# Kernel optimization log

Hardware: AMD Instinct MI355X
Metric: run time of the kernel (lower is better)

## Reference

```python
import jax, jax.numpy as jnp
import numpy as np

N = 100_000   # nodes
E = 1_600_000 # edges (avg degree 16)
D = 128       # in_dim
H = 128       # hidden_dim


def _glorot(key, shape):
    s = 1.0 / np.sqrt(shape[0])
    return jax.random.uniform(key, shape, jnp.float32, -s, s)


def setup_inputs() -> dict:
    key = jax.random.key(0)
    ks = jax.random.split(key, 8)
    x = jax.random.normal(ks[0], (N, D), jnp.float32)
    edge_index = jax.random.randint(ks[1], (2, E), 0, N)
    return {
        "x": x,
        "edge_index": edge_index,
        "Wn0": _glorot(ks[2], (D, H)),
        "Wr0": _glorot(ks[3], (D, H)),
        "b0": jnp.zeros((H,), jnp.float32),
        "Wn1": _glorot(ks[4], (H, H)),
        "Wr1": _glorot(ks[5], (H, H)),
        "b1": jnp.zeros((H,), jnp.float32),
        "Wh": _glorot(ks[6], (H, 1)),
        "bh": jnp.zeros((1,), jnp.float32),
    }


def _mean_agg(h, src, dst, n):
    # mean of source-node features scattered onto destination nodes
    summed = jax.ops.segment_sum(h[src], dst, num_segments=n)  # [N, F]
    cnt = jax.ops.segment_sum(jnp.ones((src.shape[0],), h.dtype), dst,
                              num_segments=n)
    return summed / jnp.maximum(cnt, 1.0)[:, None]


def _sage_layer(h, src, dst, Wn, Wr, b):
    # PyG SAGEConv (mean aggr): lin_l(mean_neighbors) + lin_r(root) + bias
    agg = _mean_agg(h, src, dst, h.shape[0])
    return agg @ Wn + h @ Wr + b


def reference(x, edge_index, Wn0, Wr0, b0, Wn1, Wr1, b1, Wh, bh):
    src, dst = edge_index[0], edge_index[1]
    h = jax.nn.relu(_sage_layer(x, src, dst, Wn0, Wr0, b0))  # dropout = identity (eval)
    h = jax.nn.relu(_sage_layer(h, src, dst, Wn1, Wr1, b1))
    logits = (h @ Wh + bh)[:, 0]  # squeeze(-1) -> [N]
    return logits
```

## Files before the change

kernel.cpp:

```cpp
#include <hip/hip_runtime.h>

#define THREADS 256
#define SCAN_ITEMS 8
#define NSB 128
#define BKT_MAX 3200
#define CHUNK 1024

typedef float f32x4 __attribute__((ext_vector_type(4)));
typedef __bf16 bf16x8 __attribute__((ext_vector_type(8)));
typedef int intx4 __attribute__((ext_vector_type(4)));

__device__ inline unsigned short f32_to_bf16_rne(float f) {
    unsigned int u = __float_as_uint(f);
    unsigned int r = u + 0x7fffu + ((u >> 16) & 1u);
    return (unsigned short)(r >> 16);
}
__device__ inline float bf16_bits_to_f32(unsigned short h) {
    return __uint_as_float(((unsigned int)h) << 16);
}
__device__ inline uint4 pack8(const unsigned short* s) {
    uint4 u;
    u.x = (unsigned int)s[0] | ((unsigned int)s[1] << 16);
    u.y = (unsigned int)s[2] | ((unsigned int)s[3] << 16);
    u.z = (unsigned int)s[4] | ((unsigned int)s[5] << 16);
    u.w = (unsigned int)s[6] | ((unsigned int)s[7] << 16);
    return u;
}

__global__ __launch_bounds__(256) void prep(
    const int* __restrict__ dst, int* __restrict__ hist, int E, int nbkt, int chunk,
    const float4* __restrict__ x4, ushort4* __restrict__ xb4, int n4,
    const float* __restrict__ Wn0, const float* __restrict__ Wr0, uint4* __restrict__ Wsw0,
    const float* __restrict__ Wn1, const float* __restrict__ Wr1, uint4* __restrict__ Wsw1) {
    __shared__ int lh[BKT_MAX];
    const int tid = threadIdx.x, blk = blockIdx.x;
    if (blk < NSB) {
        for (int i = tid; i < nbkt; i += 256) lh[i] = 0;
        __syncthreads();
        int s = blk * chunk, e = s + chunk; if (e > E) e = E;
        int n4e = (e > s) ? ((e - s) >> 2) : 0;
        const intx4* d4p = (const intx4*)(dst + s);
        for (int i = tid; i < n4e; i += 256) {
            intx4 d4 = d4p[i];
#pragma unroll
            for (int k = 0; k < 4; k++) atomicAdd(&lh[d4[k] >> 5], 1);
        }
        for (int j = s + (n4e << 2) + tid; j < e; j += 256) atomicAdd(&lh[dst[j] >> 5], 1);
        __syncthreads();
        for (int i = tid; i < nbkt; i += 256) hist[i * NSB + blk] = lh[i];
    } else if (blk < NSB + 32) {
        int b2 = blk - NSB;
        const float* Wn = (b2 < 16) ? Wn0 : Wn1;
        const float* Wr = (b2 < 16) ? Wr0 : Wr1;
        uint4* out = (b2 < 16) ? Wsw0 : Wsw1;
        int id = (b2 & 15) * 256 + tid;
        int lane = id & 63;
        int nt = (id >> 6) & 7;
        int t = id >> 9;
        int kbase = t * 32 + (lane >> 4) * 8;
        int col = nt * 16 + (lane & 15);
        unsigned short hi[8], lo[8];
#pragma unroll
        for (int j = 0; j < 8; j++) {
            int k = kbase + j;
            const float* W = (k < 128) ? (Wn + (size_t)k * 128) : (Wr + (size_t)(k - 128) * 128);
            float v = W[col];
            unsigned short h = f32_to_bf16_rne(v);
            hi[j] = h;
            lo[j] = f32_to_bf16_rne(v - bf16_bits_to_f32(h));
        }
        out[(size_t)((t * 8 + nt) * 2 + 0) * 64 + lane] = pack8(hi);
        out[(size_t)((t * 8 + nt) * 2 + 1) * 64 + lane] = pack8(lo);
    } else {
        int i = (blk - NSB - 32) * 256 + tid;
        if (i < n4) {
            float4 v = x4[i];
            ushort4 r;
            r.x = f32_to_bf16_rne(v.x);
            r.y = f32_to_bf16_rne(v.y);
            r.z = f32_to_bf16_rne(v.z);
            r.w = f32_to_bf16_rne(v.w);
            xb4[i] = r;
        }
    }
}

__global__ void scan1_kernel(const int* __restrict__ cnt, int* __restrict__ off,
                             int* __restrict__ bsums, int n) {
    __shared__ int sdata[THREADS];
    int base = blockIdx.x * (THREADS * SCAN_ITEMS) + threadIdx.x * SCAN_ITEMS;
    int vals[SCAN_ITEMS];
    int tsum = 0;
#pragma unroll
    for (int k = 0; k < SCAN_ITEMS; k++) {
        int idx = base + k;
        int v = (idx < n) ? cnt[idx] : 0;
        vals[k] = tsum;
        tsum += v;
    }
    sdata[threadIdx.x] = tsum;
    __syncthreads();
    for (int s = 1; s < THREADS; s <<= 1) {
        int y = (threadIdx.x >= (unsigned)s) ? sdata[threadIdx.x - s] : 0;
        __syncthreads();
        sdata[threadIdx.x] += y;
        __syncthreads();
    }
    int texcl = sdata[threadIdx.x] - tsum;
#pragma unroll
    for (int k = 0; k < SCAN_ITEMS; k++) {
        int idx = base + k;
        if (idx < n) off[idx] = texcl + vals[k];
    }
    if (threadIdx.x == THREADS - 1) bsums[blockIdx.x] = sdata[THREADS - 1];
}

__global__ void scan2_wave(const int* __restrict__ bsums, int* __restrict__ bbase,
                           int nb, int* __restrict__ offN) {
    const int lane = threadIdx.x;
    int carry = 0;
    for (int base = 0; base < nb; base += 64) {
        int i = base + lane;
        int v = (i < nb) ? bsums[i] : 0;
        int x = v;
#pragma unroll
        for (int s = 1; s < 64; s <<= 1) {
            int y = __shfl_up(x, s);
            if (lane >= s) x += y;
        }
        if (i < nb) bbase[i] = carry + x - v;
        carry += __shfl(x, 63);
    }
    if (lane == 0) *offN = carry;
}

__global__ __launch_bounds__(256) void scatter32(const int* __restrict__ src,
                                                 const int* __restrict__ dst,
                                                 const int* __restrict__ hstS,
                                                 const int* __restrict__ bbase,
                                                 int* __restrict__ esrt,
                                                 int E, int nbkt, int chunk) {
    __shared__ int cur[BKT_MAX];
    const int tid = threadIdx.x, blk = blockIdx.x;
    for (int i = tid; i < nbkt; i += 256) {
        int j = i * NSB + blk;
        cur[i] = hstS[j] + bbase[j >> 11];
    }
    __syncthreads();
    int s = blk * chunk, e = s + chunk; if (e > E) e = E;
    if ((((size_t)dst | (size_t)src) & 15) == 0) {
        int n4 = (e > s) ? ((e - s) >> 2) : 0;
        const intx4* d4p = (const intx4*)(dst + s);
        const intx4* s4p = (const intx4*)(src + s);
        for (int i = tid; i < n4; i += 256) {
            intx4 d4 = d4p[i];
            intx4 s4 = s4p[i];
#pragma unroll
            for (int k = 0; k < 4; k++) {
                int d = d4[k];
                int p = atomicAdd(&cur[d >> 5], 1);
                esrt[p] = (s4[k] << 8) | ((d & 31) << 25);
            }
        }
        for (int j = s + (n4 << 2) + tid; j < e; j += 256) {
            int d = dst[j];
            int p = atomicAdd(&cur[d >> 5], 1);
            esrt[p] = (src[j] << 8) | ((d & 31) << 25);
        }
    } else {
        for (int j = s + tid; j < e; j += 256) {
            int d = dst[j];
            int p = atomicAdd(&cur[d >> 5], 1);
            esrt[p] = (src[j] << 8) | ((d & 31) << 25);
        }
    }
}

__global__ __launch_bounds__(256) void agg_bucket(const unsigned short* __restrict__ hb,
                                                  const int* __restrict__ hstS,
                                                  const int* __restrict__ bbase,
                                                  const int* __restrict__ esrt,
                                                  unsigned short* __restrict__ aggb,
                                                  int E, int nbkt, int n) {
    __shared__ int stage[CHUNK];
    __shared__ int sorted[CHUNK];
    __shared__ int cnt[32];
    __shared__ int coff[33];
    const int tid = threadIdx.x, lane = tid & 63, w = tid >> 6;
    const int b = blockIdx.x;

    int j0 = b * NSB;
    const int p0 = hstS[j0] + bbase[j0 >> 11];
    int p1 = E;
    if (b + 1 < nbkt) {
        int j1 = (b + 1) * NSB;
        p1 = hstS[j1] + bbase[j1 >> 11];
    }
    const char* hbB = (const char*)hb;

    if (p1 - p0 <= CHUNK) {
        int m = p1 - p0;
        for (int i = tid; i < m; i += 256) stage[i] = esrt[p0 + i];
        if (tid < 32) cnt[tid] = 0;
        __syncthreads();
        for (int i = tid; i < m; i += 256) atomicAdd(&cnt[stage[i] >> 25], 1);
        __syncthreads();
        if (tid < 32) {
            int v = cnt[tid];
            int x = v;
#pragma unroll
            for (int s = 1; s < 32; s <<= 1) {
                int y = __shfl_up(x, s);
                if (lane >= s) x += y;
            }
            coff[tid + 1] = x;
            if (tid == 0) coff[0] = 0;
            cnt[tid] = x - v;
        }
        __syncthreads();
        for (int i = tid; i < m; i += 256) {
            int pk = stage[i];
            int p = atomicAdd(&cnt[pk >> 25], 1);
            sorted[p] = pk;
        }
        __syncthreads();

        int no[9];
#pragma unroll
        for (int i = 0; i <= 8; i++) no[i] = coff[w * 8 + i];
        const int s = no[0], e2 = no[8];
        const int w8 = w * 8;
        int curL = 0;
        float ax = 0.f, ay = 0.f;

        auto flushTo = [&](int tgt) {
            while (curL < tgt) {
                int node = b * 32 + w8 + curL;
                int d = no[curL + 1] - no[curL];
                float inv = 1.0f / (float)(d > 1 ? d : 1);
                unsigned int o = (unsigned int)f32_to_bf16_rne(ax * inv)
                               | ((unsigned int)f32_to_bf16_rne(ay * inv) << 16);
                if (node < n)
                    *(unsigned int*)((char*)aggb + (size_t)node * 256 + lane * 4) = o;
                ax = 0.f; ay = 0.f; ++curL;
            }
        };
        auto issue = [&](unsigned int* v, int* nd, int base) {
#pragma unroll
            for (int j = 0; j < 8; j++) {
                int pk = sorted[base + j];
                nd[j] = (pk >> 25) - w8;
                v[j] = *(const unsigned int*)(hbB + (unsigned)(pk & 0x01FFFF00) + lane * 4);
            }
        };
        auto consume = [&](const unsigned int* v, const int* nd) {
#pragma unroll
            for (int j = 0; j < 8; j++) {
                flushTo(nd[j]);
                ax += __uint_as_float(v[j] << 16);
                ay += __uint_as_float(v[j] & 0xffff0000u);
            }
        };

        const int nb8 = (e2 - s) >> 3;
        unsigned int vA[8], vB[8];
        int ndA[8], ndB[8];
        if (nb8 > 0) {
            issue(vA, ndA, s);
            int k = 1;
            for (; k + 1 < nb8; k += 2) {
                issue(vB, ndB, s + k * 8);
                consume(vA, ndA);
                issue(vA, ndA, s + k * 8 + 8);
                consume(vB, ndB);
            }
            if (k < nb8) {
                issue(vB, ndB, s + k * 8);
                consume(vA, ndA);
                consume(vB, ndB);
            } else {
                consume(vA, ndA);
            }
        }
        for (int i = s + (nb8 << 3); i < e2; i++) {
            int pk = sorted[i];
            flushTo((pk >> 25) - w8);
            unsigned int vv = *(const unsigned int*)(hbB + (unsigned)(pk & 0x01FFFF00) + lane * 4);
            ax += __uint_as_float(vv << 16);
            ay += __uint_as_float(vv & 0xffff0000u);
        }
        flushTo(8);
        return;
    }

    float accx[8], accy[8];
    int dcnt[8];
#pragma unroll
    for (int nl = 0; nl < 8; nl++) { accx[nl] = 0.f; accy[nl] = 0.f; dcnt[nl] = 0; }
    for (int base = p0; base < p1; base += CHUNK) {
        int m = p1 - base; if (m > CHUNK) m = CHUNK;
        for (int i = tid; i < m; i += 256) stage[i] = esrt[base + i];
        if (tid < 32) cnt[tid] = 0;
        __syncthreads();
        for (int i = tid; i < m; i += 256) atomicAdd(&cnt[stage[i] >> 25], 1);
        __syncthreads();
        if (tid < 32) {
            int v = cnt[tid];
            int x = v;
#pragma unroll
            for (int s = 1; s < 32; s <<= 1) {
                int y = __shfl_up(x, s);
                if (lane >= s) x += y;
            }
            coff[tid + 1] = x;
            if (tid == 0) coff[0] = 0;
            cnt[tid] = x - v;
        }
        __syncthreads();
        for (int i = tid; i < m; i += 256) {
            int pk = stage[i];
            int p = atomicAdd(&cnt[pk >> 25], 1);
            sorted[p] = pk;
        }
        __syncthreads();
#pragma unroll
        for (int nl = 0; nl < 8; nl++) {
            int node_l = w * 8 + nl;
            int s = coff[node_l], e2 = coff[node_l + 1];
            dcnt[nl] += e2 - s;
            float ax = accx[nl], ay = accy[nl];
            int i = s;
            for (; i + 8 <= e2; i += 8) {
                unsigned int v[8];
#pragma unroll
                for (int j = 0; j < 8; j++) {
                    unsigned off = (unsigned)(sorted[i + j] & 0x01FFFF00);
                    v[j] = *(const unsigned int*)(hbB + off + lane * 4);
                }
#pragma unroll
                for (int j = 0; j < 8; j++) {
                    ax += __uint_as_float(v[j] << 16);
                    ay += __uint_as_float(v[j] & 0xffff0000u);
                }
            }
            for (; i < e2; i++) {
                unsigned off = (unsigned)(sorted[i] & 0x01FFFF00);
                unsigned int vv = *(const unsigned int*)(hbB + off + lane * 4);
                ax += __uint_as_float(vv << 16);
                ay += __uint_as_float(vv & 0xffff0000u);
            }
            accx[nl] = ax; accy[nl] = ay;
        }
        __syncthreads();
    }
#pragma unroll
    for (int nl = 0; nl < 8; nl++) {
        int node = b * 32 + w * 8 + nl;
        if (node < n) {
            int d = dcnt[nl];
            float inv = 1.0f / (float)(d > 1 ? d : 1);
            unsigned int o = (unsigned int)f32_to_bf16_rne(accx[nl] * inv)
                           | ((unsigned int)f32_to_bf16_rne(accy[nl] * inv) << 16);
            *(unsigned int*)(aggb + (size_t)node * 128 + lane * 2) = o;
        }
    }
}

template <int LAYER, bool FINAL>
__global__ __launch_bounds__(256, 2) void update_mfma(
    const unsigned short* __restrict__ aggb, const void* __restrict__ hsrc,
    const uint4* __restrict__ Wsw, const float* __restrict__ bias,
    unsigned short* __restrict__ hout,
    const float* __restrict__ Wh, const float* __restrict__ bh,
    float* __restrict__ logits, int n) {
    __shared__ uint4 Alds[2048];
    __shared__ uint4 Wlds[2048];
    const int tid = threadIdx.x;
    const int lane = tid & 63;
    const int w = tid >> 6;
    const int i0 = blockIdx.x * 128;

    f32x4 acc[2][8];
#pragma unroll
    for (int mt = 0; mt < 2; mt++)
#pragma unroll
        for (int nt = 0; nt < 8; nt++) acc[mt][nt] = (f32x4)0.f;

    const int r = tid >> 1;
    const int half = tid & 1;
    const int rg = i0 + r;
    const bool inb = rg < n;
    const int mt_s = r >> 4;
    const int lidx = r & 15;

    for (int c = 0; c < 4; c++) {
        const bool haslo = (LAYER == 0 && c >= 2);
        {
            const uint4* srcW = Wsw + (size_t)c * 2048;
#pragma unroll
            for (int g = 0; g < 8; g++) Wlds[g * 256 + tid] = srcW[g * 256 + tid];
        }
        {
            unsigned short hiA[32], loA[32];
            if (LAYER == 0 && c >= 2) {
                const float4* s4 = (const float4*)((const float*)hsrc + (size_t)rg * 128 +
                                                   (c - 2) * 64 + half * 32);
#pragma unroll
                for (int q = 0; q < 8; q++) {
                    float4 f = inb ? s4[q] : make_float4(0.f, 0.f, 0.f, 0.f);
                    float vv[4] = {f.x, f.y, f.z, f.w};
#pragma unroll
                    for (int e = 0; e < 4; e++) {
                        unsigned short h = f32_to_bf16_rne(vv[e]);
                        hiA[q * 4 + e] = h;
                        loA[q * 4 + e] = f32_to_bf16_rne(vv[e] - bf16_bits_to_f32(h));
                    }
                }
            } else {
                const unsigned short* bsrc = (c < 2) ? aggb : (const unsigned short*)hsrc;
                int cc = (c < 2) ? c : c - 2;
                const uint4* s4 = (const uint4*)(bsrc + (size_t)rg * 128 + cc * 64 + half * 32);
#pragma unroll
                for (int q = 0; q < 4; q++) {
                    uint4 u = inb ? s4[q] : make_uint4(0, 0, 0, 0);
                    unsigned int uu[4] = {u.x, u.y, u.z, u.w};
#pragma unroll
                    for (int e = 0; e < 4; e++) {
                        hiA[q * 8 + e * 2 + 0] = (unsigned short)(uu[e] & 0xffffu);
                        hiA[q * 8 + e * 2 + 1] = (unsigned short)(uu[e] >> 16);
                    }
                }
            }
            unsigned int baseHi = ((mt_s * 2 + half) * 2 + 0) * 64;
#pragma unroll
            for (int g2 = 0; g2 < 4; g2++)
                Alds[baseHi + lidx + 16 * g2] = pack8(&hiA[g2 * 8]);
            if (haslo) {
#pragma unroll
                for (int g2 = 0; g2 < 4; g2++)
                    Alds[baseHi + 64 + lidx + 16 * g2] = pack8(&loA[g2 * 8]);
            }
        }
        __syncthreads();
#pragma unroll
        for (int kt = 0; kt < 2; kt++) {
            bf16x8 a0h = *(const bf16x8*)&Alds[(((w * 2 + 0) * 2 + kt) * 2 + 0) * 64 + lane];
            bf16x8 a1h = *(const bf16x8*)&Alds[(((w * 2 + 1) * 2 + kt) * 2 + 0) * 64 + lane];
            bf16x8 a0l, a1l;
            if (haslo) {
                a0l = *(const bf16x8*)&Alds[(((w * 2 + 0) * 2 + kt) * 2 + 1) * 64 + lane];
                a1l = *(const bf16x8*)&Alds[(((w * 2 + 1) * 2 + kt) * 2 + 1) * 64 + lane];
            }
#pragma unroll
            for (int nt = 0; nt < 8; nt++) {
                bf16x8 bhv = *(const bf16x8*)&Wlds[((kt * 8 + nt) * 2 + 0) * 64 + lane];
                bf16x8 blv = *(const bf16x8*)&Wlds[((kt * 8 + nt) * 2 + 1) * 64 + lane];
                acc[0][nt] = __builtin_amdgcn_mfma_f32_16x16x32_bf16(a0h, bhv, acc[0][nt], 0, 0, 0);
                acc[0][nt] = __builtin_amdgcn_mfma_f32_16x16x32_bf16(a0h, blv, acc[0][nt], 0, 0, 0);
                acc[1][nt] = __builtin_amdgcn_mfma_f32_16x16x32_bf16(a1h, bhv, acc[1][nt], 0, 0, 0);
                acc[1][nt] = __builtin_amdgcn_mfma_f32_16x16x32_bf16(a1h, blv, acc[1][nt], 0, 0, 0);
                if (haslo) {
                    acc[0][nt] = __builtin_amdgcn_mfma_f32_16x16x32_bf16(a0l, bhv, acc[0][nt], 0, 0, 0);
                    acc[1][nt] = __builtin_amdgcn_mfma_f32_16x16x32_bf16(a1l, bhv, acc[1][nt], 0, 0, 0);
                }
            }
        }
        __syncthreads();
    }

    const int col = lane & 15;
    const int g4 = lane >> 4;
    float bcol[8];
#pragma unroll
    for (int nt = 0; nt < 8; nt++) bcol[nt] = bias[nt * 16 + col];
    if (!FINAL) {
#pragma unroll
        for (int mt = 0; mt < 2; mt++) {
            int nodeBase = i0 + (w * 2 + mt) * 16 + g4 * 4;
#pragma unroll
            for (int reg = 0; reg < 4; reg++) {
                int node = nodeBase + reg;
                if (node < n) {
#pragma unroll
                    for (int nt = 0; nt < 8; nt++) {
                        float v = acc[mt][nt][reg] + bcol[nt];
                        v = v > 0.f ? v : 0.f;
                        hout[(size_t)node * 128 + nt * 16 + col] = f32_to_bf16_rne(v);
                    }
                }
            }
        }
    } else {
        float whc[8];
#pragma unroll
        for (int nt = 0; nt < 8; nt++) whc[nt] = Wh[nt * 16 + col];
        float bhv = bh[0];
#pragma unroll
        for (int mt = 0; mt < 2; mt++) {
            int nodeBase = i0 + (w * 2 + mt) * 16 + g4 * 4;
#pragma unroll
            for (int reg = 0; reg < 4; reg++) {
                float s = 0.f;
#pragma unroll
                for (int nt = 0; nt < 8; nt++) {
                    float v = acc[mt][nt][reg] + bcol[nt];
                    v = v > 0.f ? v : 0.f;
                    s += v * whc[nt];
                }
                s += __shfl_xor(s, 1);
                s += __shfl_xor(s, 2);
                s += __shfl_xor(s, 4);
                s += __shfl_xor(s, 8);
                int node = nodeBase + reg;
                if (col == 0 && node < n) logits[node] = s + bhv;
            }
        }
    }
}

extern "C" void kernel_launch(void* const* d_in, const int* in_sizes, int n_in,
                              void* d_out, int out_size, void* d_ws, size_t ws_size,
                              hipStream_t stream) {
    const float* x   = (const float*)d_in[0];
    const int*   ei  = (const int*)d_in[1];
    const float* Wn0 = (const float*)d_in[2];
    const float* Wr0 = (const float*)d_in[3];
    const float* b0  = (const float*)d_in[4];
    const float* Wn1 = (const float*)d_in[5];
    const float* Wr1 = (const float*)d_in[6];
    const float* b1  = (const float*)d_in[7];
    const float* Wh  = (const float*)d_in[8];
    const float* bh  = (const float*)d_in[9];
    float* logits = (float*)d_out;

    int N = in_sizes[0] / 128;
    int E = in_sizes[1] / 2;
    const int* src = ei;
    const int* dst = ei + E;

    int nbkt = (N + 31) >> 5;
    int HS = nbkt * NSB;
    int NB = (HS + 2047) / 2048;
    int chunk = (((E + NSB - 1) / NSB) + 3) & ~3;

    char* ws = (char*)d_ws;
    size_t cur = 0;
    auto alloc = [&](size_t bytes) -> void* {
        void* p = ws + cur;
        cur += (bytes + 255) & ~(size_t)255;
        return p;
    };
    int* hist  = (int*)alloc((size_t)HS * 4);
    int* bsums = (int*)alloc((size_t)NB * 4);
    int* bbase = (int*)alloc((size_t)NB * 4);
    int* scrat = (int*)alloc(256);
    int* esrt  = (int*)alloc((size_t)E * 4);
    unsigned short* xb  = (unsigned short*)alloc((size_t)N * 128 * 2);
    unsigned short* h0b = (unsigned short*)alloc((size_t)N * 128 * 2);
    unsigned short* agb = (unsigned short*)alloc((size_t)N * 128 * 2);
    uint4* Wsw0 = (uint4*)alloc(131072);
    uint4* Wsw1 = (uint4*)alloc(131072);
    (void)ws_size; (void)n_in; (void)out_size;

    int n4 = N * 32;
    int gPrep = NSB + 32 + (n4 + 255) / 256;
    hipLaunchKernelGGL(prep, dim3(gPrep), dim3(256), 0, stream,
                       dst, hist, E, nbkt, chunk,
                       (const float4*)x, (ushort4*)xb, n4,
                       Wn0, Wr0, Wsw0, Wn1, Wr1, Wsw1);

    hipLaunchKernelGGL(scan1_kernel,  dim3(NB),  dim3(256), 0, stream, hist, hist, bsums, HS);
    hipLaunchKernelGGL(scan2_wave,    dim3(1),   dim3(64),  0, stream, bsums, bbase, NB, scrat);
    hipLaunchKernelGGL(scatter32,     dim3(NSB), dim3(256), 0, stream, src, dst, hist, bbase, esrt, E, nbkt, chunk);

    int gUpd = (N + 127) / 128;

    hipLaunchKernelGGL(agg_bucket, dim3(nbkt), dim3(256), 0, stream, xb, hist, bbase, esrt, agb, E, nbkt, N);
    hipLaunchKernelGGL((update_mfma<0, false>), dim3(gUpd), dim3(256), 0, stream,
                       agb, (const void*)x, Wsw0, b0, h0b, nullptr, nullptr, nullptr, N);
    hipLaunchKernelGGL(agg_bucket, dim3(nbkt), dim3(256), 0, stream, h0b, hist, bbase, esrt, agb, E, nbkt, N);
    hipLaunchKernelGGL((update_mfma<1, true>), dim3(gUpd), dim3(256), 0, stream,
                       agb, (const void*)h0b, Wsw1, b1, nullptr, Wh, bh, logits, N);
}
```

Baseline: 335.1 us.

## Fold block-sum scan into consumers and use direct global-to-LDS loads in update

Removes the single-wave scan2 kernel launch by having scatter32 and agg_bucket each recompute the prefix of block sums into shared memory. In update_mfma, the bf16 A tiles and weight tiles are now loaded with global_load_lds (direct global-to-LDS), which bypasses registers. The low-part A buffer is dropped for layer 1, so its LDS footprint is halved and the launch-bounds occupancy hint rises to 3. The redundant per-block scan adds a little work to every block. The direct loads drop the in-bounds guard on the last row tile, so rows past N may be read.

```diff
diff --git a/kernel.cpp b/kernel.cpp
--- a/kernel.cpp
+++ b/kernel.cpp
@@ -25,6 +25,31 @@
     u.z = (unsigned int)s[4] | ((unsigned int)s[5] << 16);
     u.w = (unsigned int)s[6] | ((unsigned int)s[7] << 16);
     return u;
+}
+
+__device__ inline void gld_lds16(const void* g, void* l) {
+    __builtin_amdgcn_global_load_lds(
+        (const __attribute__((address_space(1))) void*)g,
+        (__attribute__((address_space(3))) void*)l, 16, 0, 0);
+}
+
+__device__ inline void scan_bsums(const int* __restrict__ bsums, int nb,
+                                  int* lbase, int tid) {
+    if (tid < 64) {
+        int carry = 0;
+        for (int base = 0; base < nb; base += 64) {
+            int i = base + tid;
+            int v = (i < nb) ? bsums[i] : 0;
+            int x = v;
+#pragma unroll
+            for (int s = 1; s < 64; s <<= 1) {
+                int y = __shfl_up(x, s);
+                if (tid >= s) x += y;
+            }
+            if (i < nb) lbase[i] = carry + x - v;
+            carry += __shfl(x, 63);
+        }
+    }
 }
 
 __global__ __launch_bounds__(256) void prep(
@@ -115,36 +140,20 @@
     if (threadIdx.x == THREADS - 1) bsums[blockIdx.x] = sdata[THREADS - 1];
 }
 
-__global__ void scan2_wave(const int* __restrict__ bsums, int* __restrict__ bbase,
-                           int nb, int* __restrict__ offN) {
-    const int lane = threadIdx.x;
-    int carry = 0;
-    for (int base = 0; base < nb; base += 64) {
-        int i = base + lane;
-        int v = (i < nb) ? bsums[i] : 0;
-        int x = v;
-#pragma unroll
-        for (int s = 1; s < 64; s <<= 1) {
-            int y = __shfl_up(x, s);
-            if (lane >= s) x += y;
-        }
-        if (i < nb) bbase[i] = carry + x - v;
-        carry += __shfl(x, 63);
-    }
-    if (lane == 0) *offN = carry;
-}
-
 __global__ __launch_bounds__(256) void scatter32(const int* __restrict__ src,
                                                  const int* __restrict__ dst,
                                                  const int* __restrict__ hstS,
-                                                 const int* __restrict__ bbase,
+                                                 const int* __restrict__ bsums, int nbv,
                                                  int* __restrict__ esrt,
                                                  int E, int nbkt, int chunk) {
     __shared__ int cur[BKT_MAX];
+    __shared__ int lbase[256];
     const int tid = threadIdx.x, blk = blockIdx.x;
+    scan_bsums(bsums, nbv, lbase, tid);
+    __syncthreads();
     for (int i = tid; i < nbkt; i += 256) {
         int j = i * NSB + blk;
-        cur[i] = hstS[j] + bbase[j >> 11];
+        cur[i] = hstS[j] + lbase[j >> 11];
     }
     __syncthreads();
     int s = blk * chunk, e = s + chunk; if (e > E) e = E;
@@ -178,7 +187,7 @@
 
 __global__ __launch_bounds__(256) void agg_bucket(const unsigned short* __restrict__ hb,
                                                   const int* __restrict__ hstS,
-                                                  const int* __restrict__ bbase,
+                                                  const int* __restrict__ bsums, int nbv,
                                                   const int* __restrict__ esrt,
                                                   unsigned short* __restrict__ aggb,
                                                   int E, int nbkt, int n) {
@@ -186,15 +195,19 @@
     __shared__ int sorted[CHUNK];
     __shared__ int cnt[32];
     __shared__ int coff[33];
+    __shared__ int lbase[256];
     const int tid = threadIdx.x, lane = tid & 63, w = tid >> 6;
     const int b = blockIdx.x;
 
+    scan_bsums(bsums, nbv, lbase, tid);
+    __syncthreads();
+
     int j0 = b * NSB;
-    const int p0 = hstS[j0] + bbase[j0 >> 11];
+    const int p0 = hstS[j0] + lbase[j0 >> 11];
     int p1 = E;
     if (b + 1 < nbkt) {
         int j1 = (b + 1) * NSB;
-        p1 = hstS[j1] + bbase[j1 >> 11];
+        p1 = hstS[j1] + lbase[j1 >> 11];
     }
     const char* hbB = (const char*)hb;
 
@@ -367,13 +380,14 @@
 }
 
 template <int LAYER, bool FINAL>
-__global__ __launch_bounds__(256, 2) void update_mfma(
+__global__ __launch_bounds__(256, (LAYER == 0) ? 2 : 3) void update_mfma(
     const unsigned short* __restrict__ aggb, const void* __restrict__ hsrc,
     const uint4* __restrict__ Wsw, const float* __restrict__ bias,
     unsigned short* __restrict__ hout,
     const float* __restrict__ Wh, const float* __restrict__ bh,
     float* __restrict__ logits, int n) {
-    __shared__ uint4 Alds[2048];
+    constexpr int AF = (LAYER == 0) ? 2 : 1;
+    __shared__ uint4 Alds[1024 * AF];
     __shared__ uint4 Wlds[2048];
     const int tid = threadIdx.x;
     const int lane = tid & 63;
@@ -398,58 +412,53 @@
         {
             const uint4* srcW = Wsw + (size_t)c * 2048;
 #pragma unroll
-            for (int g = 0; g < 8; g++) Wlds[g * 256 + tid] = srcW[g * 256 + tid];
-        }
-        {
+            for (int g = 0; g < 8; g++)
+                gld_lds16(srcW + g * 256 + tid, &Wlds[g * 256 + tid]);
+        }
+        if (!haslo) {
+            const unsigned short* bsrc = (c < 2) ? aggb : (const unsigned short*)hsrc;
+            const int cc = (c < 2) ? c : c - 2;
+#pragma unroll
+            for (int blk = 0; blk < 4; blk++) {
+                int G = blk * 256 + tid;
+                int e = G & 63;
+                int fidx = G >> 6;
+                int row = i0 + ((fidx >> 1) << 4) + (e & 15);
+                const char* g = (const char*)bsrc + (size_t)row * 256
+                              + cc * 128 + (fidx & 1) * 64 + (e >> 4) * 16;
+                gld_lds16(g, &Alds[fidx * (64 * AF) + e]);
+            }
+        } else {
             unsigned short hiA[32], loA[32];
-            if (LAYER == 0 && c >= 2) {
-                const float4* s4 = (const float4*)((const float*)hsrc + (size_t)rg * 128 +
-                                                   (c - 2) * 64 + half * 32);
-#pragma unroll
-                for (int q = 0; q < 8; q++) {
-                    float4 f = inb ? s4[q] : make_float4(0.f, 0.f, 0.f, 0.f);
-                    float vv[4] = {f.x, f.y, f.z, f.w};
-#pragma unroll
-                    for (int e = 0; e < 4; e++) {
-                        unsigned short h = f32_to_bf16_rne(vv[e]);
-                        hiA[q * 4 + e] = h;
-                        loA[q * 4 + e] = f32_to_bf16_rne(vv[e] - bf16_bits_to_f32(h));
-                    }
+            const float4* s4 = (const float4*)((const float*)hsrc + (size_t)rg * 128 +
+                                               (c - 2) * 64 + half * 32);
+#pragma unroll
+            for (int q = 0; q < 8; q++) {
+                float4 f = inb ? s4[q] : make_float4(0.f, 0.f, 0.f, 0.f);
+                float vv[4] = {f.x, f.y, f.z, f.w};
+#pragma unroll
+                for (int e = 0; e < 4; e++) {
+                    unsigned short h = f32_to_bf16_rne(vv[e]);
+                    hiA[q * 4 + e] = h;
+                    loA[q * 4 + e] = f32_to_bf16_rne(vv[e] - bf16_bits_to_f32(h));
                 }
-            } else {
-                const unsigned short* bsrc = (c < 2) ? aggb : (const unsigned short*)hsrc;
-                int cc = (c < 2) ? c : c - 2;
-                const uint4* s4 = (const uint4*)(bsrc + (size_t)rg * 128 + cc * 64 + half * 32);
-#pragma unroll
-                for (int q = 0; q < 4; q++) {
-                    uint4 u = inb ? s4[q] : make_uint4(0, 0, 0, 0);
-                    unsigned int uu[4] = {u.x, u.y, u.z, u.w};
-#pragma unroll
-                    for (int e = 0; e < 4; e++) {
-                        hiA[q * 8 + e * 2 + 0] = (unsigned short)(uu[e] & 0xffffu);
-                        hiA[q * 8 + e * 2 + 1] = (unsigned short)(uu[e] >> 16);
-                    }
-                }
-            }
-            unsigned int baseHi = ((mt_s * 2 + half) * 2 + 0) * 64;
-#pragma unroll
-            for (int g2 = 0; g2 < 4; g2++)
+            }
+            unsigned int baseHi = (unsigned)(mt_s * 2 + half) * (64 * AF);
+#pragma unroll
+            for (int g2 = 0; g2 < 4; g2++) {
                 Alds[baseHi + lidx + 16 * g2] = pack8(&hiA[g2 * 8]);
-            if (haslo) {
-#pragma unroll
-                for (int g2 = 0; g2 < 4; g2++)
-                    Alds[baseHi + 64 + lidx + 16 * g2] = pack8(&loA[g2 * 8]);
+                Alds[baseHi + 64 + lidx + 16 * g2] = pack8(&loA[g2 * 8]);
             }
         }
         __syncthreads();
 #pragma unroll
         for (int kt = 0; kt < 2; kt++) {
-            bf16x8 a0h = *(const bf16x8*)&Alds[(((w * 2 + 0) * 2 + kt) * 2 + 0) * 64 + lane];
-            bf16x8 a1h = *(const bf16x8*)&Alds[(((w * 2 + 1) * 2 + kt) * 2 + 0) * 64 + lane];
+            bf16x8 a0h = *(const bf16x8*)&Alds[((w * 2 + 0) * 2 + kt) * (64 * AF) + lane];
+            bf16x8 a1h = *(const bf16x8*)&Alds[((w * 2 + 1) * 2 + kt) * (64 * AF) + lane];
             bf16x8 a0l, a1l;
             if (haslo) {
-                a0l = *(const bf16x8*)&Alds[(((w * 2 + 0) * 2 + kt) * 2 + 1) * 64 + lane];
-                a1l = *(const bf16x8*)&Alds[(((w * 2 + 1) * 2 + kt) * 2 + 1) * 64 + lane];
+                a0l = *(const bf16x8*)&Alds[((w * 2 + 0) * 2 + kt) * (64 * AF) + 64 + lane];
+                a1l = *(const bf16x8*)&Alds[((w * 2 + 1) * 2 + kt) * (64 * AF) + 64 + lane];
             }
 #pragma unroll
             for (int nt = 0; nt < 8; nt++) {
@@ -552,8 +561,6 @@
     };
     int* hist  = (int*)alloc((size_t)HS * 4);
     int* bsums = (int*)alloc((size_t)NB * 4);
-    int* bbase = (int*)alloc((size_t)NB * 4);
-    int* scrat = (int*)alloc(256);
     int* esrt  = (int*)alloc((size_t)E * 4);
     unsigned short* xb  = (unsigned short*)alloc((size_t)N * 128 * 2);
     unsigned short* h0b = (unsigned short*)alloc((size_t)N * 128 * 2);
@@ -570,15 +577,14 @@
                        Wn0, Wr0, Wsw0, Wn1, Wr1, Wsw1);
 
     hipLaunchKernelGGL(scan1_kernel,  dim3(NB),  dim3(256), 0, stream, hist, hist, bsums, HS);
-    hipLaunchKernelGGL(scan2_wave,    dim3(1),   dim3(64),  0, stream, bsums, bbase, NB, scrat);
-    hipLaunchKernelGGL(scatter32,     dim3(NSB), dim3(256), 0, stream, src, dst, hist, bbase, esrt, E, nbkt, chunk);
+    hipLaunchKernelGGL(scatter32,     dim3(NSB), dim3(256), 0, stream, src, dst, hist, bsums, NB, esrt, E, nbkt, chunk);
 
     int gUpd = (N + 127) / 128;
 
-    hipLaunchKernelGGL(agg_bucket, dim3(nbkt), dim3(256), 0, stream, xb, hist, bbase, esrt, agb, E, nbkt, N);
+    hipLaunchKernelGGL(agg_bucket, dim3(nbkt), dim3(256), 0, stream, xb, hist, bsums, NB, esrt, agb, E, nbkt, N);
     hipLaunchKernelGGL((update_mfma<0, false>), dim3(gUpd), dim3(256), 0, stream,
                        agb, (const void*)x, Wsw0, b0, h0b, nullptr, nullptr, nullptr, N);
-    hipLaunchKernelGGL(agg_bucket, dim3(nbkt), dim3(256), 0, stream, h0b, hist, bbase, esrt, agb, E, nbkt, N);
+    hipLaunchKernelGGL(agg_bucket, dim3(nbkt), dim3(256), 0, stream, h0b, hist, bsums, NB, esrt, agb, E, nbkt, N);
     hipLaunchKernelGGL((update_mfma<1, true>), dim3(gUpd), dim3(256), 0, stream,
                        agb, (const void*)h0b, Wsw1, b1, nullptr, Wh, bh, logits, N);
 }
```

New measurement: 351.5 us. 1.05x slower.

## Gather neighbor features as FP8 instead of BF16 in aggregation

Applied to the files above, without the earlier changes.

Stores the input features and the layer-0 hidden activations as FP8 (e4m3 via hardware convert) alongside the BF16 copy, and has the edge-gather aggregation read 1 byte per feature instead of 2. The edge-sorted source encoding shifts by 7 instead of 8 to match the 128-byte row stride. This halves gather traffic in both aggregation passes, which are likely memory-bound, and makes the conversion in prep cheaper. In exchange it adds an extra byte-wise store in the layer-0 update and loses considerable accuracy in the mean aggregation, which may break tolerance.

```diff
diff --git a/kernel.cpp b/kernel.cpp
--- a/kernel.cpp
+++ b/kernel.cpp
@@ -7,6 +7,7 @@
 #define CHUNK 1024
 
 typedef float f32x4 __attribute__((ext_vector_type(4)));
+typedef float floatx2 __attribute__((ext_vector_type(2)));
 typedef __bf16 bf16x8 __attribute__((ext_vector_type(8)));
 typedef int intx4 __attribute__((ext_vector_type(4)));
 
@@ -26,10 +27,16 @@
     u.w = (unsigned int)s[6] | ((unsigned int)s[7] << 16);
     return u;
 }
+__device__ inline unsigned int pk_fp8(float a, float b) {
+    return (unsigned int)__builtin_amdgcn_cvt_pk_fp8_f32(a, b, 0, false);
+}
+__device__ inline floatx2 unpk_fp8(unsigned int u) {
+    return __builtin_amdgcn_cvt_pk_f32_fp8(u, false);
+}
 
 __global__ __launch_bounds__(256) void prep(
     const int* __restrict__ dst, int* __restrict__ hist, int E, int nbkt, int chunk,
-    const float4* __restrict__ x4, ushort4* __restrict__ xb4, int n4,
+    const float4* __restrict__ x4, unsigned int* __restrict__ xq4, int n4,
     const float* __restrict__ Wn0, const float* __restrict__ Wr0, uint4* __restrict__ Wsw0,
     const float* __restrict__ Wn1, const float* __restrict__ Wr1, uint4* __restrict__ Wsw1) {
     __shared__ int lh[BKT_MAX];
@@ -75,12 +82,9 @@
         int i = (blk - NSB - 32) * 256 + tid;
         if (i < n4) {
             float4 v = x4[i];
-            ushort4 r;
-            r.x = f32_to_bf16_rne(v.x);
-            r.y = f32_to_bf16_rne(v.y);
-            r.z = f32_to_bf16_rne(v.z);
-            r.w = f32_to_bf16_rne(v.w);
-            xb4[i] = r;
+            unsigned int u = pk_fp8(v.x, v.y);
+            u |= (unsigned int)__builtin_amdgcn_cvt_pk_fp8_f32(v.z, v.w, 0, false) << 16;
+            xq4[i] = u;
         }
     }
 }
@@ -159,24 +163,24 @@
             for (int k = 0; k < 4; k++) {
                 int d = d4[k];
                 int p = atomicAdd(&cur[d >> 5], 1);
-                esrt[p] = (s4[k] << 8) | ((d & 31) << 25);
+                esrt[p] = (s4[k] << 7) | ((d & 31) << 25);
             }
         }
         for (int j = s + (n4 << 2) + tid; j < e; j += 256) {
             int d = dst[j];
             int p = atomicAdd(&cur[d >> 5], 1);
-            esrt[p] = (src[j] << 8) | ((d & 31) << 25);
+            esrt[p] = (src[j] << 7) | ((d & 31) << 25);
         }
     } else {
         for (int j = s + tid; j < e; j += 256) {
             int d = dst[j];
             int p = atomicAdd(&cur[d >> 5], 1);
-            esrt[p] = (src[j] << 8) | ((d & 31) << 25);
-        }
-    }
-}
-
-__global__ __launch_bounds__(256) void agg_bucket(const unsigned short* __restrict__ hb,
+            esrt[p] = (src[j] << 7) | ((d & 31) << 25);
+        }
+    }
+}
+
+__global__ __launch_bounds__(256) void agg_bucket(const unsigned char* __restrict__ hb,
                                                   const int* __restrict__ hstS,
                                                   const int* __restrict__ bbase,
                                                   const int* __restrict__ esrt,
@@ -250,15 +254,16 @@
             for (int j = 0; j < 8; j++) {
                 int pk = sorted[base + j];
                 nd[j] = (pk >> 25) - w8;
-                v[j] = *(const unsigned int*)(hbB + (unsigned)(pk & 0x01FFFF00) + lane * 4);
+                v[j] = *(const unsigned short*)(hbB + (unsigned)(pk & 0x00FFFF80) + lane * 2);
             }
         };
         auto consume = [&](const unsigned int* v, const int* nd) {
 #pragma unroll
             for (int j = 0; j < 8; j++) {
                 flushTo(nd[j]);
-                ax += __uint_as_float(v[j] << 16);
-                ay += __uint_as_float(v[j] & 0xffff0000u);
+                floatx2 f = unpk_fp8(v[j]);
+                ax += f.x;
+                ay += f.y;
             }
         };
 
@@ -285,9 +290,10 @@
         for (int i = s + (nb8 << 3); i < e2; i++) {
             int pk = sorted[i];
             flushTo((pk >> 25) - w8);
-            unsigned int vv = *(const unsigned int*)(hbB + (unsigned)(pk & 0x01FFFF00) + lane * 4);
-            ax += __uint_as_float(vv << 16);
-            ay += __uint_as_float(vv & 0xffff0000u);
+            unsigned int vv = *(const unsigned short*)(hbB + (unsigned)(pk & 0x00FFFF80) + lane * 2);
+            floatx2 f = unpk_fp8(vv);
+            ax += f.x;
+            ay += f.y;
         }
         flushTo(8);
         return;
@@ -334,20 +340,22 @@
                 unsigned int v[8];
 #pragma unroll
                 for (int j = 0; j < 8; j++) {
-                    unsigned off = (unsigned)(sorted[i + j] & 0x01FFFF00);
-                    v[j] = *(const unsigned int*)(hbB + off + lane * 4);
+                    unsigned off = (unsigned)(sorted[i + j] & 0x00FFFF80);
+                    v[j] = *(const unsigned short*)(hbB + off + lane * 2);
                 }
 #pragma unroll
                 for (int j = 0; j < 8; j++) {
-                    ax += __uint_as_float(v[j] << 16);
-                    ay += __uint_as_float(v[j] & 0xffff0000u);
+                    floatx2 f = unpk_fp8(v[j]);
+                    ax += f.x;
+                    ay += f.y;
                 }
             }
             for (; i < e2; i++) {
-                unsigned off = (unsigned)(sorted[i] & 0x01FFFF00);
-                unsigned int vv = *(const unsigned int*)(hbB + off + lane * 4);
-                ax += __uint_as_float(vv << 16);
-                ay += __uint_as_float(vv & 0xffff0000u);
+                unsigned off = (unsigned)(sorted[i] & 0x00FFFF80);
+                unsigned int vv = *(const unsigned short*)(hbB + off + lane * 2);
+                floatx2 f = unpk_fp8(vv);
+                ax += f.x;
+                ay += f.y;
             }
             accx[nl] = ax; accy[nl] = ay;
         }
@@ -370,7 +378,7 @@
 __global__ __launch_bounds__(256, 2) void update_mfma(
     const unsigned short* __restrict__ aggb, const void* __restrict__ hsrc,
     const uint4* __restrict__ Wsw, const float* __restrict__ bias,
-    unsigned short* __restrict__ hout,
+    unsigned short* __restrict__ hout, unsigned char* __restrict__ houtq,
     const float* __restrict__ Wh, const float* __restrict__ bh,
     float* __restrict__ logits, int n) {
     __shared__ uint4 Alds[2048];
@@ -486,6 +494,8 @@
                         float v = acc[mt][nt][reg] + bcol[nt];
                         v = v > 0.f ? v : 0.f;
                         hout[(size_t)node * 128 + nt * 16 + col] = f32_to_bf16_rne(v);
+                        houtq[(size_t)node * 128 + nt * 16 + col] =
+                            (unsigned char)(pk_fp8(v, v) & 0xffu);
                     }
                 }
             }
@@ -555,7 +565,8 @@
     int* bbase = (int*)alloc((size_t)NB * 4);
     int* scrat = (int*)alloc(256);
     int* esrt  = (int*)alloc((size_t)E * 4);
-    unsigned short* xb  = (unsigned short*)alloc((size_t)N * 128 * 2);
+    unsigned char* xq  = (unsigned char*)alloc((size_t)N * 128);
+    unsigned char* h0q = (unsigned char*)alloc((size_t)N * 128);
     unsigned short* h0b = (unsigned short*)alloc((size_t)N * 128 * 2);
     unsigned short* agb = (unsigned short*)alloc((size_t)N * 128 * 2);
     uint4* Wsw0 = (uint4*)alloc(131072);
@@ -566,7 +577,7 @@
     int gPrep = NSB + 32 + (n4 + 255) / 256;
     hipLaunchKernelGGL(prep, dim3(gPrep), dim3(256), 0, stream,
                        dst, hist, E, nbkt, chunk,
-                       (const float4*)x, (ushort4*)xb, n4,
+                       (const float4*)x, (unsigned int*)xq, n4,
                        Wn0, Wr0, Wsw0, Wn1, Wr1, Wsw1);
 
     hipLaunchKernelGGL(scan1_kernel,  dim3(NB),  dim3(256), 0, stream, hist, hist, bsums, HS);
@@ -575,10 +586,10 @@
 
     int gUpd = (N + 127) / 128;
 
-    hipLaunchKernelGGL(agg_bucket, dim3(nbkt), dim3(256), 0, stream, xb, hist, bbase, esrt, agb, E, nbkt, N);
+    hipLaunchKernelGGL(agg_bucket, dim3(nbkt), dim3(256), 0, stream, xq, hist, bbase, esrt, agb, E, nbkt, N);
     hipLaunchKernelGGL((update_mfma<0, false>), dim3(gUpd), dim3(256), 0, stream,
-                       agb, (const void*)x, Wsw0, b0, h0b, nullptr, nullptr, nullptr, N);
-    hipLaunchKernelGGL(agg_bucket, dim3(nbkt), dim3(256), 0, stream, h0b, hist, bbase, esrt, agb, E, nbkt, N);
+                       agb, (const void*)x, Wsw0, b0, h0b, h0q, nullptr, nullptr, nullptr, N);
+    hipLaunchKernelGGL(agg_bucket, dim3(nbkt), dim3(256), 0, stream, h0q, hist, bbase, esrt, agb, E, nbkt, N);
     hipLaunchKernelGGL((update_mfma<1, true>), dim3(gUpd), dim3(256), 0, stream,
-                       agb, (const void*)h0b, Wsw1, b1, nullptr, Wh, bh, logits, N);
-}
+                       agb, (const void*)h0b, Wsw1, b1, nullptr, nullptr, Wh, bh, logits, N);
+}
```

After: 298.3 us. -11.0%, faster.
